# Kernel optimization log

Hardware: AMD Instinct MI355X
Metric: run time of the kernel (lower is better)

Reference implementation:

```python
import jax, jax.numpy as jnp
import numpy as np

B, T, C, H = 2, 512, 64, 64  # batch, seq (<= block_size), n_embd, head_size


def setup_inputs() -> dict:
    key = jax.random.key(0)
    ks = jax.random.split(key, 9)
    p = lambda k, sh: jax.random.normal(k, sh, jnp.float32) * 0.02
    return {
        "x": jax.random.normal(ks[0], (B, T, C), jnp.float32),
        "pos_emb": jax.random.normal(ks[1], (T, C), jnp.float32),
        "pos_dist_emb": jax.random.normal(ks[2], (B, T, T, 2 * C), jnp.float32),
        # GeluFeedForward(4c -> c -> 1): Linear(4c, c) -> GELU -> Linear(c, 1)
        "W1": p(ks[3], (4 * C, C)),
        "b1": p(ks[4], (C,)),
        "W2": p(ks[5], (C, 1)),
        "b2": p(ks[6], (1,)),
        # value projection Linear(c, head_size)
        "Wv": p(ks[7], (C, H)),
        "bv": p(ks[8], (H,)),
    }


def reference(x, pos_emb, pos_dist_emb, W1, b1, W2, b2, Wv, bv):
    b, t, c = x.shape
    x1 = x + pos_emb  # (b,t,c)
    # cat([k, q, pos_dist], -1) @ W1 == k@W1[:c] + q@W1[c:2c] + pd@W1[2c:]
    # (avoids materializing the (b,t,t,4c) repeat+cat tensor; same math)
    W1k, W1q, W1p = W1[:c], W1[c:2 * c], W1[2 * c:]
    kp = x1 @ W1k                 # (b,t,c): key side, varies over pair axis 2
    qp = x1 @ W1q                 # (b,t,c): query side, varies over pair axis 1
    pp = pos_dist_emb @ W1p       # (b,t,t,c)
    h = jax.nn.gelu(qp[:, :, None, :] + kp[:, None, :, :] + pp + b1,
                    approximate=False)          # (b,t,t,c)
    wei = ((h @ W2)[..., 0] + b2[0]) * (c ** -0.5)  # (b,t,t)
    causal = jnp.tril(jnp.ones((t, t), bool))
    wei = jnp.where(causal, wei, -jnp.inf)
    wei = jax.nn.softmax(wei, axis=-1)          # (b,t,t); dropout p=0
    v = x @ Wv + bv                             # (b,t,H)
    return wei @ v                              # (b,t,H)
```

## Files before the change

### kernel.cpp

```cpp
#include <hip/hip_runtime.h>
#include <math.h>

#define BB 2
#define TT 512
#define CC 64
#define HH 64
#define KK 128
#define PADK 136
#define JT 64

typedef __attribute__((ext_vector_type(8))) short short8;
typedef __attribute__((ext_vector_type(4))) float float4v;

__device__ inline unsigned short f2bf(float f) {
    unsigned int u = __float_as_uint(f);
    u = (u + 0x7FFFu + ((u >> 16) & 1u)) >> 16;
    return (unsigned short)u;
}

__global__ __launch_bounds__(256) void pack_kernel(
    const float* __restrict__ W1, unsigned short* __restrict__ Wpt)
{
    int t = blockIdx.x * 256 + threadIdx.x;
    int c = t >> 7;
    int k = t & 127;
    Wpt[c * PADK + k] = f2bf(W1[(2 * CC + k) * CC + c]);
}

__global__ __launch_bounds__(64) void prep_kernel(
    const float* __restrict__ x, const float* __restrict__ pos_emb,
    const float* __restrict__ W1, const float* __restrict__ b1,
    const float* __restrict__ Wv, const float* __restrict__ bv,
    float* __restrict__ kp, float* __restrict__ qpb, float* __restrict__ v)
{
    const int row = blockIdx.x;
    const int t = row & (TT - 1);
    const int c = threadIdx.x;
    __shared__ float xs[CC], x1s[CC];
    float xv = x[row * CC + c];
    xs[c] = xv;
    x1s[c] = xv + pos_emb[t * CC + c];
    __syncthreads();
    float ak = 0.f, aq = 0.f, av = 0.f;
#pragma unroll 8
    for (int k = 0; k < CC; ++k) {
        ak = fmaf(x1s[k], W1[k * CC + c], ak);
        aq = fmaf(x1s[k], W1[(CC + k) * CC + c], aq);
        av = fmaf(xs[k], Wv[k * HH + c], av);
    }
    kp[row * CC + c] = ak;
    qpb[row * CC + c] = aq + b1[c];
    v[row * HH + c] = av + bv[c];
}

__global__ __launch_bounds__(256) void wei_kernel(
    const float* __restrict__ pd, const unsigned short* __restrict__ Wpt,
    const float* __restrict__ W2, const float* __restrict__ b2,
    const float* __restrict__ kp, const float* __restrict__ qpb,
    float* __restrict__ wei)
{
    const int i = blockIdx.y;
    const int b = blockIdx.z;
    const int j0 = blockIdx.x * JT;
    if (j0 > i) return;

    __shared__ unsigned short Alds[JT * PADK];
    __shared__ unsigned short Blds[CC * PADK];

    const int tid = threadIdx.x;

    {
        const uint4* __restrict__ src = (const uint4*)Wpt;
        uint4* dst = (uint4*)Blds;
#pragma unroll
        for (int f = 0; f < 5; ++f) {
            int idx = f * 256 + tid;
            if (idx < (CC * PADK) / 8) dst[idx] = src[idx];
        }
    }

    {
        const float4* __restrict__ p4 =
            (const float4*)(pd + (((size_t)b * TT + i) * TT + j0) * KK);
#pragma unroll
        for (int it = 0; it < 8; ++it) {
            int f = it * 256 + tid;
            float4 val = p4[f];
            int j = f >> 5;
            int kq = f & 31;
            uint2 u;
            u.x = (unsigned)f2bf(val.x) | ((unsigned)f2bf(val.y) << 16);
            u.y = (unsigned)f2bf(val.z) | ((unsigned)f2bf(val.w) << 16);
            *(uint2*)&Alds[j * PADK + kq * 4] = u;
        }
    }
    __syncthreads();

    const int wave = tid >> 6;
    const int lane = tid & 63;
    const int m = lane & 15;
    const int kg = lane >> 4;

    float4v acc[4] = {{0.f,0.f,0.f,0.f},{0.f,0.f,0.f,0.f},
                      {0.f,0.f,0.f,0.f},{0.f,0.f,0.f,0.f}};
    const int arow = wave * 16 + m;
#pragma unroll
    for (int kt = 0; kt < 4; ++kt) {
        short8 a = *(const short8*)&Alds[arow * PADK + kt * 32 + kg * 8];
#pragma unroll
        for (int nt = 0; nt < 4; ++nt) {
            short8 bf = *(const short8*)&Blds[(nt * 16 + m) * PADK + kt * 32 + kg * 8];
            acc[nt] = __builtin_amdgcn_mfma_f32_16x16x32_bf16(a, bf, acc[nt], 0, 0, 0);
        }
    }

    float w2v[4], qv[4];
#pragma unroll
    for (int nt = 0; nt < 4; ++nt) {
        int c = nt * 16 + m;
        w2v[nt] = W2[c];
        qv[nt] = qpb[((size_t)b * TT + i) * CC + c];
    }
    const float b2v = b2[0];

#pragma unroll
    for (int r = 0; r < 4; ++r) {
        const int j = j0 + wave * 16 + kg * 4 + r;
        float s = 0.f;
#pragma unroll
        for (int nt = 0; nt < 4; ++nt) {
            float tv = acc[nt][r] + qv[nt] + kp[((size_t)b * TT + j) * CC + nt * 16 + m];
            float g = 0.5f * tv * (1.f + erff(tv * 0.70710678118654752f));
            s = fmaf(g, w2v[nt], s);
        }
#pragma unroll
        for (int off = 1; off < 16; off <<= 1) s += __shfl_xor(s, off);
        if (m == r && j <= i)
            wei[((size_t)b * TT + i) * TT + j] = (s + b2v) * 0.125f;
    }
}

__device__ inline float wave_reduce_max(float m) {
#pragma unroll
    for (int off = 32; off > 0; off >>= 1) m = fmaxf(m, __shfl_down(m, off));
    return m;
}
__device__ inline float wave_reduce_sum(float s) {
#pragma unroll
    for (int off = 32; off > 0; off >>= 1) s += __shfl_down(s, off);
    return s;
}

__global__ __launch_bounds__(256) void out_kernel(
    const float* __restrict__ wei, const float* __restrict__ v,
    float* __restrict__ out)
{
    const int i = blockIdx.x;
    const int b = blockIdx.y;
    const int tid = threadIdx.x;
    const int wv = tid >> 6;
    const int lane = tid & 63;
    const int n = i + 1;

    __shared__ float p[TT];
    __shared__ float red[4];
    __shared__ float part[4][HH];

    float m = -1e30f;
    for (int jj = tid; jj < n; jj += 256) {
        float w = wei[((size_t)b * TT + i) * TT + jj];
        p[jj] = w;
        m = fmaxf(m, w);
    }
    m = wave_reduce_max(m);
    if (lane == 0) red[wv] = m;
    __syncthreads();
    const float M = fmaxf(fmaxf(red[0], red[1]), fmaxf(red[2], red[3]));
    __syncthreads();

    float s = 0.f;
    for (int jj = tid; jj < n; jj += 256) {
        float e = __expf(p[jj] - M);
        p[jj] = e;
        s += e;
    }
    s = wave_reduce_sum(s);
    if (lane == 0) red[wv] = s;
    __syncthreads();
    const float S = red[0] + red[1] + red[2] + red[3];
    const float inv = 1.f / S;

    float acc = 0.f, acc2 = 0.f;
    int jj = wv;
    for (; jj + 4 < n; jj += 8) {
        acc  = fmaf(p[jj],     v[((size_t)b * TT + jj) * HH + lane], acc);
        acc2 = fmaf(p[jj + 4], v[((size_t)b * TT + jj + 4) * HH + lane], acc2);
    }
    if (jj < n)
        acc = fmaf(p[jj], v[((size_t)b * TT + jj) * HH + lane], acc);
    acc += acc2;
    part[wv][lane] = acc;
    __syncthreads();
    if (tid < HH) {
        float r = (part[0][tid] + part[1][tid] + part[2][tid] + part[3][tid]) * inv;
        out[((size_t)b * TT + i) * HH + tid] = r;
    }
}

extern "C" void kernel_launch(void* const* d_in, const int* in_sizes, int n_in,
                              void* d_out, int out_size, void* d_ws, size_t ws_size,
                              hipStream_t stream)
{
    const float* x       = (const float*)d_in[0];
    const float* pos_emb = (const float*)d_in[1];
    const float* pd      = (const float*)d_in[2];
    const float* W1      = (const float*)d_in[3];
    const float* b1      = (const float*)d_in[4];
    const float* W2      = (const float*)d_in[5];
    const float* b2      = (const float*)d_in[6];
    const float* Wv      = (const float*)d_in[7];
    const float* bv      = (const float*)d_in[8];
    float* out = (float*)d_out;

    float* ws = (float*)d_ws;
    unsigned short* Wpt = (unsigned short*)ws;
    float* kp  = ws + 4608;
    float* qpb = ws + 4608 + 65536;
    float* v   = ws + 4608 + 131072;
    float* wei = ws + 4608 + 196608;

    pack_kernel<<<dim3(32), dim3(256), 0, stream>>>(W1, Wpt);
    prep_kernel<<<dim3(BB * TT), dim3(64), 0, stream>>>(x, pos_emb, W1, b1, Wv, bv, kp, qpb, v);
    wei_kernel<<<dim3(TT / JT, TT, BB), dim3(256), 0, stream>>>(pd, Wpt, W2, b2, kp, qpb, wei);
    out_kernel<<<dim3(TT, BB), dim3(256), 0, stream>>>(wei, v, out);
}
```

Before: 404.8 us.

## Load MFMA operands directly from global memory instead of staging through LDS

The wei kernel no longer stages the pos_dist tile and packed W1 slice in shared memory. Each lane now loads its A fragment straight from global memory as float4s, converts to bf16 in registers, and reads B fragments directly from the packed weight buffer, which drops the row padding. This removes LDS traffic and the block barrier, and lowers LDS usage, which may raise occupancy, at the cost of less coalesced global reads and repeated weight loads served through cache. The out kernel's P·V loop is also unrolled to four accumulators.

```diff
diff --git a/kernel.cpp b/kernel.cpp
--- a/kernel.cpp
+++ b/kernel.cpp
@@ -6,7 +6,6 @@
 #define CC 64
 #define HH 64
 #define KK 128
-#define PADK 136
 #define JT 64
 
 typedef __attribute__((ext_vector_type(8))) short short8;
@@ -18,13 +17,22 @@
     return (unsigned short)u;
 }
 
+__device__ inline short8 cvt8(float4 a, float4 b) {
+    short8 r;
+    r[0] = (short)f2bf(a.x); r[1] = (short)f2bf(a.y);
+    r[2] = (short)f2bf(a.z); r[3] = (short)f2bf(a.w);
+    r[4] = (short)f2bf(b.x); r[5] = (short)f2bf(b.y);
+    r[6] = (short)f2bf(b.z); r[7] = (short)f2bf(b.w);
+    return r;
+}
+
 __global__ __launch_bounds__(256) void pack_kernel(
     const float* __restrict__ W1, unsigned short* __restrict__ Wpt)
 {
     int t = blockIdx.x * 256 + threadIdx.x;
     int c = t >> 7;
     int k = t & 127;
-    Wpt[c * PADK + k] = f2bf(W1[(2 * CC + k) * CC + c]);
+    Wpt[c * KK + k] = f2bf(W1[(2 * CC + k) * CC + c]);
 }
 
 __global__ __launch_bounds__(64) void prep_kernel(
@@ -64,52 +72,31 @@
     const int j0 = blockIdx.x * JT;
     if (j0 > i) return;
 
-    __shared__ unsigned short Alds[JT * PADK];
-    __shared__ unsigned short Blds[CC * PADK];
-
     const int tid = threadIdx.x;
-
-    {
-        const uint4* __restrict__ src = (const uint4*)Wpt;
-        uint4* dst = (uint4*)Blds;
-#pragma unroll
-        for (int f = 0; f < 5; ++f) {
-            int idx = f * 256 + tid;
-            if (idx < (CC * PADK) / 8) dst[idx] = src[idx];
-        }
-    }
-
-    {
-        const float4* __restrict__ p4 =
-            (const float4*)(pd + (((size_t)b * TT + i) * TT + j0) * KK);
-#pragma unroll
-        for (int it = 0; it < 8; ++it) {
-            int f = it * 256 + tid;
-            float4 val = p4[f];
-            int j = f >> 5;
-            int kq = f & 31;
-            uint2 u;
-            u.x = (unsigned)f2bf(val.x) | ((unsigned)f2bf(val.y) << 16);
-            u.y = (unsigned)f2bf(val.z) | ((unsigned)f2bf(val.w) << 16);
-            *(uint2*)&Alds[j * PADK + kq * 4] = u;
-        }
-    }
-    __syncthreads();
-
     const int wave = tid >> 6;
     const int lane = tid & 63;
     const int m = lane & 15;
     const int kg = lane >> 4;
 
+    const int jrow = j0 + wave * 16 + m;
+    const float* __restrict__ arow =
+        pd + (((size_t)b * TT + i) * TT + jrow) * KK + kg * 8;
+
+    float4 av[8];
+#pragma unroll
+    for (int kt = 0; kt < 4; ++kt) {
+        av[2 * kt]     = *(const float4*)(arow + kt * 32);
+        av[2 * kt + 1] = *(const float4*)(arow + kt * 32 + 4);
+    }
+
     float4v acc[4] = {{0.f,0.f,0.f,0.f},{0.f,0.f,0.f,0.f},
                       {0.f,0.f,0.f,0.f},{0.f,0.f,0.f,0.f}};
-    const int arow = wave * 16 + m;
 #pragma unroll
     for (int kt = 0; kt < 4; ++kt) {
-        short8 a = *(const short8*)&Alds[arow * PADK + kt * 32 + kg * 8];
+        short8 a = cvt8(av[2 * kt], av[2 * kt + 1]);
 #pragma unroll
         for (int nt = 0; nt < 4; ++nt) {
-            short8 bf = *(const short8*)&Blds[(nt * 16 + m) * PADK + kt * 32 + kg * 8];
+            short8 bf = *(const short8*)&Wpt[(nt * 16 + m) * KK + kt * 32 + kg * 8];
             acc[nt] = __builtin_amdgcn_mfma_f32_16x16x32_bf16(a, bf, acc[nt], 0, 0, 0);
         }
     }
@@ -190,16 +177,17 @@
     const float S = red[0] + red[1] + red[2] + red[3];
     const float inv = 1.f / S;
 
-    float acc = 0.f, acc2 = 0.f;
+    float a0 = 0.f, a1 = 0.f, a2 = 0.f, a3 = 0.f;
     int jj = wv;
-    for (; jj + 4 < n; jj += 8) {
-        acc  = fmaf(p[jj],     v[((size_t)b * TT + jj) * HH + lane], acc);
-        acc2 = fmaf(p[jj + 4], v[((size_t)b * TT + jj + 4) * HH + lane], acc2);
-    }
-    if (jj < n)
-        acc = fmaf(p[jj], v[((size_t)b * TT + jj) * HH + lane], acc);
-    acc += acc2;
-    part[wv][lane] = acc;
+    for (; jj + 12 < n; jj += 16) {
+        a0 = fmaf(p[jj],      v[((size_t)b * TT + jj) * HH + lane], a0);
+        a1 = fmaf(p[jj + 4],  v[((size_t)b * TT + jj + 4) * HH + lane], a1);
+        a2 = fmaf(p[jj + 8],  v[((size_t)b * TT + jj + 8) * HH + lane], a2);
+        a3 = fmaf(p[jj + 12], v[((size_t)b * TT + jj + 12) * HH + lane], a3);
+    }
+    for (; jj < n; jj += 4)
+        a0 = fmaf(p[jj], v[((size_t)b * TT + jj) * HH + lane], a0);
+    part[wv][lane] = a0 + a1 + a2 + a3;
     __syncthreads();
     if (tid < HH) {
         float r = (part[0][tid] + part[1][tid] + part[2][tid] + part[3][tid]) * inv;
@@ -224,10 +212,10 @@
 
     float* ws = (float*)d_ws;
     unsigned short* Wpt = (unsigned short*)ws;
-    float* kp  = ws + 4608;
-    float* qpb = ws + 4608 + 65536;
-    float* v   = ws + 4608 + 131072;
-    float* wei = ws + 4608 + 196608;
+    float* kp  = ws + 4096;
+    float* qpb = ws + 4096 + 65536;
+    float* v   = ws + 4096 + 131072;
+    float* wei = ws + 4096 + 196608;
 
     pack_kernel<<<dim3(32), dim3(256), 0, stream>>>(W1, Wpt);
     prep_kernel<<<dim3(BB * TT), dim3(64), 0, stream>>>(x, pos_emb, W1, b1, Wv, bv, kp, qpb, v);
```

Result: slower. 423.6 us (+4.7%).
